# Kernel optimization log

Measured on AMD Instinct MI355X. Metric: run time of the kernel, lower is better.

The kernel has to match this reference:

```python
import jax, jax.numpy as jnp
import numpy as np

B, H, W, DIM, NH, WS, SS = 32, 56, 56, 512, 16, 7, 3
L = H * W
HD = DIM // NH
N = WS * WS
SCALE = HD ** -0.5
EPS = 1e-5


def _rel_pos_index():
    coords = np.stack(np.meshgrid(np.arange(WS), np.arange(WS), indexing='ij'))  # (2,ws,ws)
    cf = coords.reshape(2, -1)
    rc = (cf[:, :, None] - cf[:, None, :]).transpose(1, 2, 0).astype(np.int64)  # (N,N,2)
    rc[..., 0] += WS - 1
    rc[..., 1] += WS - 1
    rc[..., 0] *= 2 * WS - 1
    return rc.sum(-1)  # (N,N)


def _shift_mask():
    img = np.zeros((H, W), np.float32)
    cnt = 0
    for hs in (slice(0, -WS), slice(-WS, -SS), slice(-SS, None)):
        for ws_ in (slice(0, -WS), slice(-WS, -SS), slice(-SS, None)):
            img[hs, ws_] = cnt
            cnt += 1
    m = img.reshape(H // WS, WS, W // WS, WS).transpose(0, 2, 1, 3).reshape(-1, N)  # (nW,N)
    diff = m[:, None, :] - m[:, :, None]
    return np.where(diff != 0, -100.0, 0.0).astype(np.float32)  # (nW,N,N)


REL_IDX = jnp.asarray(_rel_pos_index())
ATTN_MASK = jnp.asarray(_shift_mask())


def _ln(x, g, b):
    mu = jnp.mean(x, -1, keepdims=True)
    var = jnp.var(x, -1, keepdims=True)
    return (x - mu) * jax.lax.rsqrt(var + EPS) * g + b


def setup_inputs() -> dict:
    key = jax.random.key(0)
    ks = jax.random.split(key, 8)
    s = 0.02
    return {
        'x': jax.random.normal(ks[0], (B, L, DIM), jnp.float32),
        'norm1_g': jnp.ones((DIM,), jnp.float32),
        'norm1_b': jnp.zeros((DIM,), jnp.float32),
        'qkv_w': jax.random.normal(ks[1], (DIM, 3 * DIM), jnp.float32) * s,
        'qkv_b': jnp.zeros((3 * DIM,), jnp.float32),
        'rel_bias_table': jax.random.normal(ks[2], ((2 * WS - 1) ** 2, NH), jnp.float32) * s,
        'proj_w': jax.random.normal(ks[3], (DIM, DIM), jnp.float32) * s,
        'proj_b': jnp.zeros((DIM,), jnp.float32),
        'norm2_g': jnp.ones((DIM,), jnp.float32),
        'norm2_b': jnp.zeros((DIM,), jnp.float32),
        'fc1_w': jax.random.normal(ks[4], (DIM, 4 * DIM), jnp.float32) * s,
        'fc1_b': jnp.zeros((4 * DIM,), jnp.float32),
        'fc2_w': jax.random.normal(ks[5], (4 * DIM, DIM), jnp.float32) * s,
        'fc2_b': jnp.zeros((DIM,), jnp.float32),
    }


def reference(x, norm1_g, norm1_b, qkv_w, qkv_b, rel_bias_table, proj_w, proj_b,
              norm2_g, norm2_b, fc1_w, fc1_b, fc2_w, fc2_b):
    shortcut = x
    h = _ln(x, norm1_g, norm1_b).reshape(B, H, W, DIM)
    # cyclic shift
    h = jnp.roll(h, (-SS, -SS), axis=(1, 2))
    # window partition -> (B*nW, N, C)
    nWh, nWw = H // WS, W // WS
    h = h.reshape(B, nWh, WS, nWw, WS, DIM).transpose(0, 1, 3, 2, 4, 5).reshape(-1, N, DIM)
    Bw = h.shape[0]
    # qkv
    qkv = (h @ qkv_w + qkv_b).reshape(Bw, N, 3, NH, HD).transpose(2, 0, 3, 1, 4)
    q, k, v = qkv[0], qkv[1], qkv[2]  # (Bw, NH, N, HD)
    attn = jnp.einsum('bhnd,bhmd->bhnm', q * SCALE, k)
    # relative position bias (NH, N, N)
    bias = rel_bias_table[REL_IDX.reshape(-1)].reshape(N, N, NH).transpose(2, 0, 1)
    attn = attn + bias[None]
    # shift mask: (B, nW, NH, N, N) + (1, nW, 1, N, N)
    nW = nWh * nWw
    attn = attn.reshape(B, nW, NH, N, N) + ATTN_MASK[None, :, None]
    attn = jax.nn.softmax(attn.reshape(Bw, NH, N, N), axis=-1)
    out = jnp.einsum('bhnm,bhmd->bhnd', attn, v).transpose(0, 2, 1, 3).reshape(Bw, N, DIM)
    out = out @ proj_w + proj_b
    # window reverse + reverse shift
    out = out.reshape(B, nWh, nWw, WS, WS, DIM).transpose(0, 1, 3, 2, 4, 5).reshape(B, H, W, DIM)
    out = jnp.roll(out, (SS, SS), axis=(1, 2)).reshape(B, L, DIM)
    x = shortcut + out
    # MLP (GELU exact, matching torch nn.GELU default)
    y = _ln(x, norm2_g, norm2_b)
    y = jax.nn.gelu(y @ fc1_w + fc1_b, approximate=False) @ fc2_w + fc2_b
    return x + y
```

## Files before the change

kernel.cpp:

```cpp
#include <hip/hip_runtime.h>
#include <hip/hip_bf16.h>
#include <math.h>

#define MROWS 100352
#define MHALF 50176
#define DIM   512
#define LL    3136
#define HH    56
#define SSH   3
#define SCALE_QK 0.17677669529663687f

typedef __bf16 bf16;
typedef __bf16 bf16x8 __attribute__((ext_vector_type(8)));
typedef __bf16 bf16x4 __attribute__((ext_vector_type(4)));
typedef float  f32x4  __attribute__((ext_vector_type(4)));

typedef __attribute__((address_space(1))) void* gas_ptr;
typedef __attribute__((address_space(3))) void* las_ptr;

__device__ __forceinline__ void gload_lds16(const void* g, void* l) {
  __builtin_amdgcn_global_load_lds((gas_ptr)g, (las_ptr)l, 16, 0, 0);
}

__device__ __forceinline__ int nat_row(int r) {
  int bw = r / 49;
  int n  = r - bw * 49;
  int b  = bw >> 6;
  int wh = (bw >> 3) & 7;
  int ww = bw & 7;
  int i  = n / 7;
  int j  = n - i * 7;
  int hs = wh * 7 + i + SSH; if (hs >= HH) hs -= HH;
  int ws = ww * 7 + j + SSH; if (ws >= HH) ws -= HH;
  return b * LL + hs * HH + ws;
}

__global__ __launch_bounds__(256) void tcast_kernel(const float* __restrict__ src,
                                                    bf16* __restrict__ dst,
                                                    int Kd, int Nd) {
  __shared__ float t[32][33];
  int tx = threadIdx.x & 31, ty = threadIdx.x >> 5;
  int n0 = blockIdx.x * 32, k0 = blockIdx.y * 32;
  #pragma unroll
  for (int yy = ty; yy < 32; yy += 8)
    t[yy][tx] = src[(size_t)(k0 + yy) * Nd + n0 + tx];
  __syncthreads();
  #pragma unroll
  for (int yy = ty; yy < 32; yy += 8)
    dst[(size_t)(n0 + yy) * Kd + k0 + tx] = (bf16)t[tx][yy];
}

__global__ __launch_bounds__(256) void biasM_kernel(const float* __restrict__ table,
                                                    float* __restrict__ biasM) {
  int e = blockIdx.x * 256 + threadIdx.x;
  if (e >= 4 * 16 * 2401) return;
  int k  = e % 49;
  int t  = e / 49;
  int qv = t % 49; t /= 49;
  int head = t & 15;
  int cls  = t >> 4;
  int i1 = qv / 7, j1 = qv - i1 * 7;
  int i2 = k / 7,  j2 = k - i2 * 7;
  float b = table[((i1 - i2 + 6) * 13 + (j1 - j2 + 6)) * 16 + head];
  int labq = ((cls & 2) ? ((i1 < 4) ? 1 : 2) : 0) * 3 + ((cls & 1) ? ((j1 < 4) ? 1 : 2) : 0);
  int labk = ((cls & 2) ? ((i2 < 4) ? 1 : 2) : 0) * 3 + ((cls & 1) ? ((j2 < 4) ? 1 : 2) : 0);
  biasM[e] = b + ((labq == labk) ? 0.f : -100.f);
}

template<int PERM>
__global__ __launch_bounds__(256) void ln_kernel(const float* __restrict__ x,
                                                 const float* __restrict__ gw,
                                                 const float* __restrict__ bw_,
                                                 bf16* __restrict__ out) {
  int wave = threadIdx.x >> 6, lane = threadIdx.x & 63;
  int r = blockIdx.x * 4 + wave;
  int src = PERM ? nat_row(r) : r;
  const float* px = x + (size_t)src * DIM + lane * 8;
  float4 v0 = *(const float4*)px;
  float4 v1 = *(const float4*)(px + 4);
  float s = v0.x + v0.y + v0.z + v0.w + v1.x + v1.y + v1.z + v1.w;
  float q = v0.x*v0.x + v0.y*v0.y + v0.z*v0.z + v0.w*v0.w
          + v1.x*v1.x + v1.y*v1.y + v1.z*v1.z + v1.w*v1.w;
  #pragma unroll
  for (int m = 1; m < 64; m <<= 1) { s += __shfl_xor(s, m); q += __shfl_xor(q, m); }
  float mean = s * (1.f / DIM);
  float var  = q * (1.f / DIM) - mean * mean;
  float rstd = rsqrtf(var + 1e-5f);
  int c0 = lane * 8;
  float4 g0 = *(const float4*)(gw + c0),  g1 = *(const float4*)(gw + c0 + 4);
  float4 b0 = *(const float4*)(bw_ + c0), b1 = *(const float4*)(bw_ + c0 + 4);
  bf16x8 o;
  o[0] = (bf16)((v0.x - mean) * rstd * g0.x + b0.x);
  o[1] = (bf16)((v0.y - mean) * rstd * g0.y + b0.y);
  o[2] = (bf16)((v0.z - mean) * rstd * g0.z + b0.z);
  o[3] = (bf16)((v0.w - mean) * rstd * g0.w + b0.w);
  o[4] = (bf16)((v1.x - mean) * rstd * g1.x + b1.x);
  o[5] = (bf16)((v1.y - mean) * rstd * g1.y + b1.y);
  o[6] = (bf16)((v1.z - mean) * rstd * g1.z + b1.z);
  o[7] = (bf16)((v1.w - mean) * rstd * g1.w + b1.w);
  *(bf16x8*)(out + (size_t)r * DIM + c0) = o;
}


#define MF(a,b,c) __builtin_amdgcn_mfma_f32_16x16x32_bf16((a),(b),(c),0,0,0)
#define BAR() __builtin_amdgcn_s_barrier()
#define WLG() asm volatile("s_waitcnt lgkmcnt(0)" ::: "memory")
#define WVM(n) asm volatile("s_waitcnt vmcnt(" #n ")" ::: "memory")

template<int MODE, int KD, int ND>
__global__ __launch_bounds__(512, 2) void gemm256_kernel(const bf16* __restrict__ A,
                                                         const bf16* __restrict__ Bt,
                                                         const float* __restrict__ bias,
                                                         const float* __restrict__ resid,
                                                         bf16* __restrict__ outB,
                                                         float* __restrict__ outF,
                                                         bf16* __restrict__ outK,
                                                         bf16* __restrict__ outV) {
  constexpr int NTN = ND / 256;
  constexpr int NI  = KD / 128;
  __shared__ bf16 lds[65536];

  const int tid = threadIdx.x, lane = tid & 63, wv = tid >> 6;
  const int lr = lane & 15, lg = lane >> 4;
  const int wm = wv >> 2, wn = wv & 3;

  int nwg = gridDim.x, orig = blockIdx.x;
  int q = nwg >> 3, r = nwg & 7, xcd = orig & 7;
  int wgid = (xcd < r ? xcd * (q + 1) : r * (q + 1) + (xcd - r) * q) + (orig >> 3);
  int tm = wgid / NTN, tn = wgid % NTN;

  const bf16* gA = A  + (size_t)tm * 256 * KD;
  const bf16* gB = Bt + (size_t)tn * 256 * KD;

  const int klg  = (lg * 8) ^ ((lr & 8) ? 16 : 0);
  const int a_rd = (wm * 128 + lr) * 32 + klg;
  const int b_rd = (wn * 64 + lr) * 32 + klg;

  const int kbOffE = (wv >> 2) * 8192;
  const int kGlob  = (wv >> 2) * 32 + (((lane & 3) * 8) ^ ((lane & 32) ? 16 : 0));
  const int rl0    = ((wv * 2) & 7) * 16 + (lane >> 2);
  const int rl1    = rl0 + 16;
  const int c0off  = ((wv * 2) & 7) * 512;

#define STG(GP, DB, h, koff) \
  gload_lds16((GP) + (size_t)((h) * 128 + rl0) * KD + (koff) + kGlob, \
              (void*)(lds + (DB) + kbOffE + (h) * 4096 + c0off)); \
  gload_lds16((GP) + (size_t)((h) * 128 + rl1) * KD + (koff) + kGlob, \
              (void*)(lds + (DB) + kbOffE + (h) * 4096 + c0off + 512));

  f32x4 acc[8][4];
  #pragma unroll
  for (int i = 0; i < 8; i++)
    #pragma unroll
    for (int j = 0; j < 4; j++) { acc[i][j][0]=0.f; acc[i][j][1]=0.f; acc[i][j][2]=0.f; acc[i][j][3]=0.f; }

  bf16x8 Af[4][2], Bf0[2][2], Bf1[2][2];

  STG(gA, 0,     0, 0)  STG(gA, 0,     1, 0)
  STG(gB, 16384, 0, 0)  STG(gB, 16384, 1, 0)
  STG(gA, 32768, 0, 64) STG(gA, 32768, 1, 64)
  STG(gB, 49152, 0, 64) STG(gB, 49152, 1, 64)
  WVM(8); BAR();

#define PHASES(AB, BB, DOST, KST, ENDW) { \
    _Pragma("unroll") for (int m = 0; m < 4; m++) { \
      Af[m][0] = *(const bf16x8*)(lds + (AB) + m * 512 + a_rd); \
      Af[m][1] = *(const bf16x8*)(lds + (AB) + 8192 + m * 512 + a_rd); } \
    _Pragma("unroll") for (int n = 0; n < 2; n++) { \
      Bf0[n][0] = *(const bf16x8*)(lds + (BB) + n * 512 + b_rd); \
      Bf0[n][1] = *(const bf16x8*)(lds + (BB) + 8192 + n * 512 + b_rd); } \
    BAR(); WLG(); __builtin_amdgcn_s_setprio(1); \
    _Pragma("unroll") for (int m = 0; m < 4; m++) \
      _Pragma("unroll") for (int n = 0; n < 2; n++) { \
        acc[m][n] = MF(Af[m][0], Bf0[n][0], acc[m][n]); \
        acc[m][n] = MF(Af[m][1], Bf0[n][1], acc[m][n]); } \
    __builtin_amdgcn_s_setprio(0); BAR(); \
    _Pragma("unroll") for (int n = 0; n < 2; n++) { \
      Bf1[n][0] = *(const bf16x8*)(lds + (BB) + (n + 2) * 512 + b_rd); \
      Bf1[n][1] = *(const bf16x8*)(lds + (BB) + 8192 + (n + 2) * 512 + b_rd); } \
    if (DOST) { STG(gB, (BB), 0, (KST)) } \
    BAR(); WLG(); __builtin_amdgcn_s_setprio(1); \
    _Pragma("unroll") for (int m = 0; m < 4; m++) \
      _Pragma("unroll") for (int n = 0; n < 2; n++) { \
        acc[m][n + 2] = MF(Af[m][0], Bf1[n][0], acc[m][n + 2]); \
        acc[m][n + 2] = MF(Af[m][1], Bf1[n][1], acc[m][n + 2]); } \
    __builtin_amdgcn_s_setprio(0); BAR(); \
    _Pragma("unroll") for (int m = 0; m < 4; m++) { \
      Af[m][0] = *(const bf16x8*)(lds + (AB) + (m + 4) * 512 + a_rd); \
      Af[m][1] = *(const bf16x8*)(lds + (AB) + 8192 + (m + 4) * 512 + a_rd); } \
    if (DOST) { STG(gB, (BB), 1, (KST)) STG(gA, (AB), 0, (KST)) } \
    BAR(); WLG(); __builtin_amdgcn_s_setprio(1); \
    _Pragma("unroll") for (int m = 0; m < 4; m++) \
      _Pragma("unroll") for (int n = 0; n < 2; n++) { \
        acc[m + 4][n + 2] = MF(Af[m][0], Bf1[n][0], acc[m + 4][n + 2]); \
        acc[m + 4][n + 2] = MF(Af[m][1], Bf1[n][1], acc[m + 4][n + 2]); } \
    __builtin_amdgcn_s_setprio(0); BAR(); \
    if (DOST) { STG(gA, (AB), 1, (KST)) } \
    BAR(); WLG(); __builtin_amdgcn_s_setprio(1); \
    _Pragma("unroll") for (int m = 0; m < 4; m++) \
      _Pragma("unroll") for (int n = 0; n < 2; n++) { \
        acc[m + 4][n] = MF(Af[m][0], Bf0[n][0], acc[m + 4][n]); \
        acc[m + 4][n] = MF(Af[m][1], Bf0[n][1], acc[m + 4][n]); } \
    __builtin_amdgcn_s_setprio(0); ENDW; BAR(); \
  }

  #pragma unroll 1
  for (int I = 0; I < NI - 1; ++I) {
    int ke = (2 * I + 2) * 64;
    PHASES(0,     16384, 1, ke,      WVM(6));
    PHASES(32768, 49152, 1, ke + 64, WVM(6));
  }
  PHASES(0,     16384, 0, 0, WVM(0));
  PHASES(32768, 49152, 0, 0, ((void)0));

#undef PHASES
#undef STG

  #pragma unroll
  for (int fm = 0; fm < 8; fm++) {
    #pragma unroll
    for (int rr = 0; rr < 4; rr++) {
      int row = tm * 256 + wm * 128 + fm * 16 + lg * 4 + rr;
      int orow = (MODE == 1) ? nat_row(row) : row;
      int win = 0, nn = 0;
      if (MODE == 4) { win = row / 49; nn = row - win * 49; }
      #pragma unroll
      for (int fn = 0; fn < 4; fn++) {
        int col = tn * 256 + wn * 64 + fn * 16 + lr;
        float v = acc[fm][fn][rr] + bias[col];
        if (MODE == 1) {
          outF[(size_t)orow * ND + col] = resid[(size_t)orow * ND + col] + v;
        } else if (MODE == 2) {
          float g = 0.5f * v * (1.f + erff(v * 0.70710678118654752f));
          outB[(size_t)row * ND + col] = (bf16)g;
        } else if (MODE == 3) {
          outF[(size_t)row * ND + col] = resid[(size_t)row * ND + col] + v;
        } else if (MODE == 4) {
          int c = col & 511;
          int head = c >> 5, d = c & 31;
          size_t sb = (size_t)(win * 16 + head) * 1568 + nn * 32 + d;
          if (col < 512)        outB[sb] = (bf16)v;
          else if (col < 1024)  outK[sb] = (bf16)v;
          else                  outV[sb] = (bf16)v;
        }
      }
    }
  }
}

__global__ __launch_bounds__(256) void attn_kernel(const bf16* __restrict__ Qb,
                                                   const bf16* __restrict__ Kb,
                                                   const bf16* __restrict__ Vb,
                                                   const float* __restrict__ biasM,
                                                   bf16* __restrict__ attnO) {
  __shared__ bf16 P[4][64 * 72];
  __shared__ bf16 Vs[4][49 * 36];
  int wave = threadIdx.x >> 6, lane = threadIdx.x & 63;
  int lr = lane & 15, lg = lane >> 4;
  int wid = blockIdx.x * 4 + wave;
  int win = wid >> 4, head = wid & 15;
  int wh = (win >> 3) & 7, ww = win & 7;
  int cls = ((wh == 7) ? 2 : 0) | ((ww == 7) ? 1 : 0);
  const bf16* qp = Qb + (size_t)wid * 1568;
  const bf16* kp = Kb + (size_t)wid * 1568;
  const bf16* vp = Vb + (size_t)wid * 1568;
  const float* bp = biasM + (size_t)cls * 38416 + head * 2401;

  for (int i = lane; i < 196; i += 64) {
    bf16x8 v = *(const bf16x8*)(vp + i * 8);
    int nn = i >> 2, d = (i & 3) * 8;
    ((bf16x4*)(&Vs[wave][nn * 36 + d]))[0] = ((bf16x4*)&v)[0];
    ((bf16x4*)(&Vs[wave][nn * 36 + d + 4]))[0] = ((bf16x4*)&v)[1];
  }

  f32x4 zero4 = {0.f, 0.f, 0.f, 0.f};
  bf16x8 aq[4], bk[4];
  #pragma unroll
  for (int mi = 0; mi < 4; mi++) {
    int qq = mi * 16 + lr; if (qq > 48) qq = 48;
    aq[mi] = *(const bf16x8*)(qp + qq * 32 + lg * 8);
    bk[mi] = *(const bf16x8*)(kp + qq * 32 + lg * 8);
  }
  f32x4 sacc[4][4];
  #pragma unroll
  for (int mi = 0; mi < 4; mi++)
    #pragma unroll
    for (int ni = 0; ni < 4; ni++)
      sacc[mi][ni] = __builtin_amdgcn_mfma_f32_16x16x32_bf16(aq[mi], bk[ni], zero4, 0, 0, 0);

  float rsum[4][4];
  #pragma unroll
  for (int mi = 0; mi < 4; mi++) {
    #pragma unroll
    for (int rr = 0; rr < 4; rr++) {
      int qrow = mi * 16 + lg * 4 + rr;
      int qc = qrow > 48 ? 48 : qrow;
      const float* bq = bp + qc * 49;
      float pv[4];
      float mv = -3.0e30f;
      #pragma unroll
      for (int ni = 0; ni < 4; ni++) {
        int key = ni * 16 + lr;
        float v = (key < 49) ? sacc[mi][ni][rr] * SCALE_QK + bq[key] : -1e30f;
        pv[ni] = v;
        mv = fmaxf(mv, v);
      }
      #pragma unroll
      for (int m = 1; m < 16; m <<= 1) mv = fmaxf(mv, __shfl_xor(mv, m));
      float sum = 0.f;
      #pragma unroll
      for (int ni = 0; ni < 4; ni++) {
        float p = __expf(pv[ni] - mv);
        sum += p;
        P[wave][qrow * 72 + ni * 16 + lr] = (bf16)p;
      }
      #pragma unroll
      for (int m = 1; m < 16; m <<= 1) sum += __shfl_xor(sum, m);
      rsum[mi][rr] = sum;
    }
  }
  __syncthreads();

  f32x4 oacc[4][2];
  #pragma unroll
  for (int mi = 0; mi < 4; mi++) { oacc[mi][0] = zero4; oacc[mi][1] = zero4; }
  #pragma unroll
  for (int ks = 0; ks < 2; ks++) {
    bf16x8 bv[2];
    #pragma unroll
    for (int n2 = 0; n2 < 2; n2++)
      #pragma unroll
      for (int j = 0; j < 8; j++) {
        int kv = ks * 32 + lg * 8 + j;
        if (kv > 48) kv = 48;
        bv[n2][j] = Vs[wave][kv * 36 + n2 * 16 + lr];
      }
    #pragma unroll
    for (int mi = 0; mi < 4; mi++) {
      bf16x8 ap = *(const bf16x8*)(&P[wave][(mi * 16 + lr) * 72 + ks * 32 + lg * 8]);
      #pragma unroll
      for (int n2 = 0; n2 < 2; n2++)
        oacc[mi][n2] = __builtin_amdgcn_mfma_f32_16x16x32_bf16(ap, bv[n2], oacc[mi][n2], 0, 0, 0);
    }
  }
  #pragma unroll
  for (int mi = 0; mi < 4; mi++) {
    #pragma unroll
    for (int rr = 0; rr < 4; rr++) {
      int qrow = mi * 16 + lg * 4 + rr;
      if (qrow < 49) {
        float inv = 1.f / rsum[mi][rr];
        #pragma unroll
        for (int n2 = 0; n2 < 2; n2++)
          attnO[((size_t)win * 49 + qrow) * DIM + head * 32 + n2 * 16 + lr] =
              (bf16)(oacc[mi][n2][rr] * inv);
      }
    }
  }
}

extern "C" void kernel_launch(void* const* d_in, const int* in_sizes, int n_in,
                              void* d_out, int out_size, void* d_ws, size_t ws_size,
                              hipStream_t stream) {
  const float* x      = (const float*)d_in[0];
  const float* n1g    = (const float*)d_in[1];
  const float* n1b    = (const float*)d_in[2];
  const float* qkv_w  = (const float*)d_in[3];
  const float* qkv_b  = (const float*)d_in[4];
  const float* tabl   = (const float*)d_in[5];
  const float* proj_w = (const float*)d_in[6];
  const float* proj_b = (const float*)d_in[7];
  const float* n2g    = (const float*)d_in[8];
  const float* n2b    = (const float*)d_in[9];
  const float* fc1_w  = (const float*)d_in[10];
  const float* fc1_b  = (const float*)d_in[11];
  const float* fc2_w  = (const float*)d_in[12];
  const float* fc2_b  = (const float*)d_in[13];
  float* out = (float*)d_out;

  char* ws = (char*)d_ws;
  bf16*  RegA   = (bf16*)ws;
  bf16*  Qb     = (bf16*)(ws + 102760448);
  bf16*  Kb     = (bf16*)(ws + 102760448 + 102760448);
  bf16*  RegB   = Qb;
  char*  reg2   = ws + 308281344;
  bf16*  Vb     = (bf16*)reg2;
  float* biasM  = (float*)(reg2 + 102760448);
  float* x2     = (float*)reg2;
  bf16*  qkvWt  = (bf16*)(ws + 308281344 + 205520896);
  bf16*  projWt = qkvWt + 1536 * 512;
  bf16*  fc1Wt  = projWt + 512 * 512;
  bf16*  fc2Wt  = fc1Wt + 2048 * 512;

  biasM_kernel<<<(4 * 16 * 2401 + 255) / 256, 256, 0, stream>>>(tabl, biasM);
  tcast_kernel<<<dim3(1536 / 32, 512 / 32), 256, 0, stream>>>(qkv_w, qkvWt, 512, 1536);
  tcast_kernel<<<dim3(512 / 32, 512 / 32), 256, 0, stream>>>(proj_w, projWt, 512, 512);
  tcast_kernel<<<dim3(2048 / 32, 512 / 32), 256, 0, stream>>>(fc1_w, fc1Wt, 512, 2048);
  tcast_kernel<<<dim3(512 / 32, 2048 / 32), 256, 0, stream>>>(fc2_w, fc2Wt, 2048, 512);

  ln_kernel<1><<<MROWS / 4, 256, 0, stream>>>(x, n1g, n1b, RegA);
  gemm256_kernel<4, 512, 1536><<<(MROWS / 256) * 6, 512, 0, stream>>>(
      RegA, qkvWt, qkv_b, nullptr, Qb, nullptr, Kb, Vb);
  attn_kernel<<<2048 * 16 / 4, 256, 0, stream>>>(Qb, Kb, Vb, biasM, RegA);
  gemm256_kernel<1, 512, 512><<<(MROWS / 256) * 2, 512, 0, stream>>>(
      RegA, projWt, proj_b, x, nullptr, x2, nullptr, nullptr);
  ln_kernel<0><<<MROWS / 4, 256, 0, stream>>>(x2, n2g, n2b, RegA);
  for (int c = 0; c < 2; ++c) {
    const bf16* a1 = RegA + (size_t)c * MHALF * 512;
    gemm256_kernel<2, 512, 2048><<<(MHALF / 256) * 8, 512, 0, stream>>>(
        a1, fc1Wt, fc1_b, nullptr, RegB, nullptr, nullptr, nullptr);
    gemm256_kernel<3, 2048, 512><<<(MHALF / 256) * 2, 512, 0, stream>>>(
        RegB, fc2Wt, fc2_b, x2 + (size_t)c * MHALF * 512, nullptr,
        out + (size_t)c * MHALF * 512, nullptr, nullptr);
  }
}
```

Baseline: 1.744 ms.

## Stage GEMM epilogue through swizzled LDS for vectorized stores; keep residual x2 in bf16

Each GEMM epilogue now writes bias-added (and GELU-applied) results into a swizzled LDS tile and then re-reads them as 16-byte rows, so global stores become coalesced bf16x8 writes instead of scattered 2-byte and 4-byte stores. The intermediate residual x2 is stored as bf16 rather than fp32, which halves its write traffic and the reads done by LN2 and the fc2 epilogue. The cost is an extra LDS round trip and barriers in the epilogue, plus lower precision on the residual stream, which could raise output error.

New measurement: 1.618 ms. 1.08x faster.

```diff
diff --git a/kernel.cpp b/kernel.cpp
--- a/kernel.cpp
+++ b/kernel.cpp
@@ -33,6 +33,10 @@
   int hs = wh * 7 + i + SSH; if (hs >= HH) hs -= HH;
   int ws = ww * 7 + j + SSH; if (ws >= HH) ws -= HH;
   return b * LL + hs * HH + ws;
+}
+
+__device__ __forceinline__ int swz(int row, int colB) {
+  return (row * 512 + colB) ^ (((row >> 2) & 3) << 5);
 }
 
 __global__ __launch_bounds__(256) void tcast_kernel(const float* __restrict__ src,
@@ -67,20 +71,28 @@
   biasM[e] = b + ((labq == labk) ? 0.f : -100.f);
 }
 
-template<int PERM>
-__global__ __launch_bounds__(256) void ln_kernel(const float* __restrict__ x,
+template<int PERM, int BF16IN>
+__global__ __launch_bounds__(256) void ln_kernel(const void* __restrict__ xin,
                                                  const float* __restrict__ gw,
                                                  const float* __restrict__ bw_,
                                                  bf16* __restrict__ out) {
   int wave = threadIdx.x >> 6, lane = threadIdx.x & 63;
   int r = blockIdx.x * 4 + wave;
   int src = PERM ? nat_row(r) : r;
-  const float* px = x + (size_t)src * DIM + lane * 8;
-  float4 v0 = *(const float4*)px;
-  float4 v1 = *(const float4*)(px + 4);
-  float s = v0.x + v0.y + v0.z + v0.w + v1.x + v1.y + v1.z + v1.w;
-  float q = v0.x*v0.x + v0.y*v0.y + v0.z*v0.z + v0.w*v0.w
-          + v1.x*v1.x + v1.y*v1.y + v1.z*v1.z + v1.w*v1.w;
+  float f[8];
+  if (BF16IN) {
+    bf16x8 vv = *(const bf16x8*)((const bf16*)xin + (size_t)src * DIM + lane * 8);
+    #pragma unroll
+    for (int j = 0; j < 8; j++) f[j] = (float)vv[j];
+  } else {
+    const float* px = (const float*)xin + (size_t)src * DIM + lane * 8;
+    float4 v0 = *(const float4*)px;
+    float4 v1 = *(const float4*)(px + 4);
+    f[0]=v0.x; f[1]=v0.y; f[2]=v0.z; f[3]=v0.w; f[4]=v1.x; f[5]=v1.y; f[6]=v1.z; f[7]=v1.w;
+  }
+  float s = 0.f, q = 0.f;
+  #pragma unroll
+  for (int j = 0; j < 8; j++) { s += f[j]; q += f[j] * f[j]; }
   #pragma unroll
   for (int m = 1; m < 64; m <<= 1) { s += __shfl_xor(s, m); q += __shfl_xor(q, m); }
   float mean = s * (1.f / DIM);
@@ -89,15 +101,11 @@
   int c0 = lane * 8;
   float4 g0 = *(const float4*)(gw + c0),  g1 = *(const float4*)(gw + c0 + 4);
   float4 b0 = *(const float4*)(bw_ + c0), b1 = *(const float4*)(bw_ + c0 + 4);
+  float gg[8] = {g0.x,g0.y,g0.z,g0.w,g1.x,g1.y,g1.z,g1.w};
+  float bb[8] = {b0.x,b0.y,b0.z,b0.w,b1.x,b1.y,b1.z,b1.w};
   bf16x8 o;
-  o[0] = (bf16)((v0.x - mean) * rstd * g0.x + b0.x);
-  o[1] = (bf16)((v0.y - mean) * rstd * g0.y + b0.y);
-  o[2] = (bf16)((v0.z - mean) * rstd * g0.z + b0.z);
-  o[3] = (bf16)((v0.w - mean) * rstd * g0.w + b0.w);
-  o[4] = (bf16)((v1.x - mean) * rstd * g1.x + b1.x);
-  o[5] = (bf16)((v1.y - mean) * rstd * g1.y + b1.y);
-  o[6] = (bf16)((v1.z - mean) * rstd * g1.z + b1.z);
-  o[7] = (bf16)((v1.w - mean) * rstd * g1.w + b1.w);
+  #pragma unroll
+  for (int j = 0; j < 8; j++) o[j] = (bf16)((f[j] - mean) * rstd * gg[j] + bb[j]);
   *(bf16x8*)(out + (size_t)r * DIM + c0) = o;
 }
 
@@ -111,7 +119,8 @@
 __global__ __launch_bounds__(512, 2) void gemm256_kernel(const bf16* __restrict__ A,
                                                          const bf16* __restrict__ Bt,
                                                          const float* __restrict__ bias,
-                                                         const float* __restrict__ resid,
+                                                         const float* __restrict__ residF,
+                                                         const bf16* __restrict__ residB,
                                                          bf16* __restrict__ outB,
                                                          float* __restrict__ outF,
                                                          bf16* __restrict__ outK,
@@ -216,34 +225,62 @@
 #undef PHASES
 #undef STG
 
-  #pragma unroll
-  for (int fm = 0; fm < 8; fm++) {
-    #pragma unroll
-    for (int rr = 0; rr < 4; rr++) {
-      int row = tm * 256 + wm * 128 + fm * 16 + lg * 4 + rr;
-      int orow = (MODE == 1) ? nat_row(row) : row;
-      int win = 0, nn = 0;
-      if (MODE == 4) { win = row / 49; nn = row - win * 49; }
-      #pragma unroll
-      for (int fn = 0; fn < 4; fn++) {
-        int col = tn * 256 + wn * 64 + fn * 16 + lr;
-        float v = acc[fm][fn][rr] + bias[col];
-        if (MODE == 1) {
-          outF[(size_t)orow * ND + col] = resid[(size_t)orow * ND + col] + v;
-        } else if (MODE == 2) {
-          float g = 0.5f * v * (1.f + erff(v * 0.70710678118654752f));
-          outB[(size_t)row * ND + col] = (bf16)g;
-        } else if (MODE == 3) {
-          outF[(size_t)row * ND + col] = resid[(size_t)row * ND + col] + v;
-        } else if (MODE == 4) {
-          int c = col & 511;
-          int head = c >> 5, d = c & 31;
-          size_t sb = (size_t)(win * 16 + head) * 1568 + nn * 32 + d;
-          if (col < 512)        outB[sb] = (bf16)v;
-          else if (col < 1024)  outK[sb] = (bf16)v;
-          else                  outV[sb] = (bf16)v;
-        }
+  char* ldsb = (char*)lds;
+  float bias4[4];
+  #pragma unroll
+  for (int fn = 0; fn < 4; fn++) bias4[fn] = bias[tn * 256 + wn * 64 + fn * 16 + lr];
+  __syncthreads();
+  #pragma unroll
+  for (int fm = 0; fm < 8; fm++)
+    #pragma unroll
+    for (int fn = 0; fn < 4; fn++)
+      #pragma unroll
+      for (int rr = 0; rr < 4; rr++) {
+        int row = wm * 128 + fm * 16 + lg * 4 + rr;
+        int colB = (wn * 64 + fn * 16 + lr) * 2;
+        float v = acc[fm][fn][rr] + bias4[fn];
+        if (MODE == 2) v = 0.5f * v * (1.f + erff(v * 0.70710678118654752f));
+        *(bf16*)(ldsb + swz(row, colB)) = (bf16)v;
       }
+  __syncthreads();
+
+  const int lrow = tid >> 5, cu = tid & 31;
+  bf16* dst4 = nullptr;
+  if (MODE == 4) {
+    int third = (tn * 256) >> 9;
+    dst4 = third == 0 ? outB : (third == 1 ? outK : outV);
+  }
+  #pragma unroll 4
+  for (int s = 0; s < 16; s++) {
+    int row = s * 16 + lrow;
+    bf16x8 v = *(const bf16x8*)(ldsb + swz(row, cu * 16));
+    int grow = tm * 256 + row;
+    int gcol = tn * 256 + cu * 8;
+    if (MODE == 2) {
+      *(bf16x8*)(outB + (size_t)grow * ND + gcol) = v;
+    } else if (MODE == 1) {
+      int orow = nat_row(grow);
+      const float* rp = residF + (size_t)orow * 512 + gcol;
+      float4 r0 = *(const float4*)rp, r1 = *(const float4*)(rp + 4);
+      bf16x8 o;
+      o[0] = (bf16)(r0.x + (float)v[0]); o[1] = (bf16)(r0.y + (float)v[1]);
+      o[2] = (bf16)(r0.z + (float)v[2]); o[3] = (bf16)(r0.w + (float)v[3]);
+      o[4] = (bf16)(r1.x + (float)v[4]); o[5] = (bf16)(r1.y + (float)v[5]);
+      o[6] = (bf16)(r1.z + (float)v[6]); o[7] = (bf16)(r1.w + (float)v[7]);
+      *(bf16x8*)(outB + (size_t)orow * 512 + gcol) = o;
+    } else if (MODE == 3) {
+      bf16x8 rb = *(const bf16x8*)(residB + (size_t)grow * 512 + gcol);
+      float4 o0, o1;
+      o0.x = (float)rb[0] + (float)v[0]; o0.y = (float)rb[1] + (float)v[1];
+      o0.z = (float)rb[2] + (float)v[2]; o0.w = (float)rb[3] + (float)v[3];
+      o1.x = (float)rb[4] + (float)v[4]; o1.y = (float)rb[5] + (float)v[5];
+      o1.z = (float)rb[6] + (float)v[6]; o1.w = (float)rb[7] + (float)v[7];
+      float* op = outF + (size_t)grow * 512 + gcol;
+      *(float4*)op = o0; *(float4*)(op + 4) = o1;
+    } else {
+      int win = grow / 49, nn = grow - win * 49;
+      int head = (gcol >> 5) & 15, d = gcol & 31;
+      *(bf16x8*)(dst4 + (size_t)(win * 16 + head) * 1568 + nn * 32 + d) = v;
     }
   }
 }
@@ -385,8 +422,8 @@
   bf16*  RegB   = Qb;
   char*  reg2   = ws + 308281344;
   bf16*  Vb     = (bf16*)reg2;
+  bf16*  x2b    = (bf16*)reg2;
   float* biasM  = (float*)(reg2 + 102760448);
-  float* x2     = (float*)reg2;
   bf16*  qkvWt  = (bf16*)(ws + 308281344 + 205520896);
   bf16*  projWt = qkvWt + 1536 * 512;
   bf16*  fc1Wt  = projWt + 512 * 512;
@@ -398,19 +435,19 @@
   tcast_kernel<<<dim3(2048 / 32, 512 / 32), 256, 0, stream>>>(fc1_w, fc1Wt, 512, 2048);
   tcast_kernel<<<dim3(512 / 32, 2048 / 32), 256, 0, stream>>>(fc2_w, fc2Wt, 2048, 512);
 
-  ln_kernel<1><<<MROWS / 4, 256, 0, stream>>>(x, n1g, n1b, RegA);
+  ln_kernel<1, 0><<<MROWS / 4, 256, 0, stream>>>((const void*)x, n1g, n1b, RegA);
   gemm256_kernel<4, 512, 1536><<<(MROWS / 256) * 6, 512, 0, stream>>>(
-      RegA, qkvWt, qkv_b, nullptr, Qb, nullptr, Kb, Vb);
+      RegA, qkvWt, qkv_b, nullptr, nullptr, Qb, nullptr, Kb, Vb);
   attn_kernel<<<2048 * 16 / 4, 256, 0, stream>>>(Qb, Kb, Vb, biasM, RegA);
   gemm256_kernel<1, 512, 512><<<(MROWS / 256) * 2, 512, 0, stream>>>(
-      RegA, projWt, proj_b, x, nullptr, x2, nullptr, nullptr);
-  ln_kernel<0><<<MROWS / 4, 256, 0, stream>>>(x2, n2g, n2b, RegA);
+      RegA, projWt, proj_b, x, nullptr, x2b, nullptr, nullptr, nullptr);
+  ln_kernel<0, 1><<<MROWS / 4, 256, 0, stream>>>((const void*)x2b, n2g, n2b, RegA);
   for (int c = 0; c < 2; ++c) {
     const bf16* a1 = RegA + (size_t)c * MHALF * 512;
     gemm256_kernel<2, 512, 2048><<<(MHALF / 256) * 8, 512, 0, stream>>>(
-        a1, fc1Wt, fc1_b, nullptr, RegB, nullptr, nullptr, nullptr);
+        a1, fc1Wt, fc1_b, nullptr, nullptr, RegB, nullptr, nullptr, nullptr);
     gemm256_kernel<3, 2048, 512><<<(MHALF / 256) * 2, 512, 0, stream>>>(
-        RegB, fc2Wt, fc2_b, x2 + (size_t)c * MHALF * 512, nullptr,
+        RegB, fc2Wt, fc2_b, nullptr, x2b + (size_t)c * MHALF * 512, nullptr,
         out + (size_t)c * MHALF * 512, nullptr, nullptr);
   }
 }
```
